# Performance work log

Hardware: AMD Instinct MI355X
Metric: run time of the kernel (lower is better)

The kernel has to match this reference:

```python
import jax, jax.numpy as jnp
import numpy as np

N, IN_DIM, H1, D, K, E, HEADS = 4096, 3000, 512, 64, 32, 49152, 4
ATT_THRESH = 0.25


def setup_inputs() -> dict:
    key = jax.random.key(0)
    ks = jax.random.split(key, 20)
    glorot = lambda k, fi, fo: jax.random.normal(k, (fi, fo), jnp.float32) * (2.0 / (fi + fo)) ** 0.5
    return {
        "x": jax.random.normal(ks[0], (N, IN_DIM), jnp.float32),
        "edge_index": jax.random.randint(ks[1], (2, E), 0, N, jnp.int32),
        "sub_nodes": jax.random.randint(ks[2], (N, K), 0, N, jnp.int32),
        # GCN encoder: in_dim -> 512 -> 64
        "enc_w1": glorot(ks[3], IN_DIM, H1), "enc_b1": jnp.zeros((H1,), jnp.float32),
        "enc_w2": glorot(ks[4], H1, D), "enc_b2": jnp.zeros((D,), jnp.float32),
        # linear decoder: 64 -> 512 -> in_dim
        "dec_w1": glorot(ks[5], D, H1), "dec_b1": jnp.zeros((H1,), jnp.float32),
        "dec_w2": glorot(ks[6], H1, IN_DIM), "dec_b2": jnp.zeros((IN_DIM,), jnp.float32),
        # MultiheadAttention (torch layout: in_proj_weight [3D, D], out_proj.weight [D, D])
        "attn_in_w": jax.random.normal(ks[7], (3 * D, D), jnp.float32) * (2.0 / D) ** 0.5,
        "attn_in_b": jnp.zeros((3 * D,), jnp.float32),
        "attn_out_w": jax.random.normal(ks[8], (D, D), jnp.float32) * (2.0 / D) ** 0.5,
        "attn_out_b": jnp.zeros((D,), jnp.float32),
        # Bilinear discriminator
        "bil_w": glorot(ks[9], D, D), "bil_b": jnp.zeros((), jnp.float32),
    }


def _gcn_conv(x, src, dst, W, b):
    n = x.shape[0]
    deg = jax.ops.segment_sum(jnp.ones(src.shape, x.dtype), dst, num_segments=n) + 1.0
    inv = jax.lax.rsqrt(deg)
    h = x @ W  # [n, out]
    coef = (inv[src] * inv[dst])[:, None]
    agg = jax.ops.segment_sum(h[src] * coef, dst, num_segments=n)
    agg = agg + h * (inv * inv)[:, None]  # self-loop contribution
    return agg + b


def _mha(x, in_w, in_b, out_w, out_b):
    # x: [N, D]; torch MultiheadAttention with batch of 1, dropout=0
    n, d = x.shape
    dh = d // HEADS
    qkv = x @ in_w.T + in_b  # [N, 3D]
    q, k, v = jnp.split(qkv, 3, axis=-1)
    rs = lambda t: t.reshape(n, HEADS, dh).transpose(1, 0, 2)  # [H, N, dh]
    q, k, v = rs(q), rs(k), rs(v)
    scores = jnp.einsum("hnd,hmd->hnm", q, k) / jnp.sqrt(jnp.asarray(dh, x.dtype))
    attn = jax.nn.softmax(scores, axis=-1)  # [H, N, N]
    out = jnp.einsum("hnm,hmd->hnd", attn, v).transpose(1, 0, 2).reshape(n, d)
    out = out @ out_w.T + out_b
    return out, attn.mean(axis=0)  # averaged attn weights [N, N]


def reference(x, edge_index, sub_nodes,
              enc_w1, enc_b1, enc_w2, enc_b2,
              dec_w1, dec_b1, dec_w2, dec_b2,
              attn_in_w, attn_in_b, attn_out_w, attn_out_b,
              bil_w, bil_b):
    src, dst = edge_index[0], edge_index[1]
    # GCN encoder
    h = jax.nn.relu(_gcn_conv(x, src, dst, enc_w1, enc_b1))
    spot_emb = _gcn_conv(h, src, dst, enc_w2, enc_b2)  # [N, D]
    # per-node subgraph gather + mean pool (global_mean_pool over fixed-size niches)
    local_niches = spot_emb[sub_nodes].mean(axis=1)  # [N, D]
    # linear decoder
    recon = jax.nn.relu(local_niches @ dec_w1 + dec_b1) @ dec_w2 + dec_b2
    # self-attention over all spots
    global_niches, attn_w = _mha(local_niches, attn_in_w, attn_in_b, attn_out_w, attn_out_b)
    # low-attention negative sampling
    n = local_niches.shape[0]
    kk = int(n * ATT_THRESH)
    _, idx = jax.lax.top_k(-attn_w, kk)  # smallest-k per row
    rand_idx = jax.random.randint(jax.random.key(42), (n,), 0, kk)
    sampled = idx[jnp.arange(n), rand_idx]
    neg_global = global_niches[sampled]
    # bilinear discriminator logits
    logits_pos = jnp.einsum("nd,de,ne->n", local_niches, bil_w, global_niches) + bil_b
    logits_neg = jnp.einsum("nd,de,ne->n", local_niches, bil_w, neg_global) + bil_b
    return recon, logits_pos, logits_neg
```

## Files before the change

### kernel.cpp

```cpp
#include <hip/hip_runtime.h>
#include <hip/hip_bf16.h>
#include <stdint.h>

#define NN      4096
#define INDIM   3000
#define H1DIM   512
#define DDIM    64
#define RECON_ELEMS (NN * INDIM)

typedef __attribute__((ext_vector_type(8))) __bf16          bf16x8;
typedef __attribute__((ext_vector_type(8))) unsigned short  u16x8;
typedef __attribute__((ext_vector_type(4))) float           f32x4;
typedef __attribute__((ext_vector_type(4))) unsigned int    u32x4;

__device__ __forceinline__ unsigned short f2bf(float f) {
  union { float f; unsigned int i; } v; v.f = f;
  unsigned int x = v.i;
  unsigned int lsb = (x >> 16) & 1u;
  x += 0x7FFFu + lsb;
  return (unsigned short)(x >> 16);
}

__device__ __forceinline__ void tf2x32(unsigned k0, unsigned k1, unsigned x0, unsigned x1,
                                       unsigned &o0, unsigned &o1) {
  unsigned ks2 = k0 ^ k1 ^ 0x1BD11BDAu;
  x0 += k0; x1 += k1;
#define TFR(r) { x0 += x1; x1 = (x1 << (r)) | (x1 >> (32 - (r))); x1 ^= x0; }
  TFR(13) TFR(15) TFR(26) TFR(6)
  x0 += k1; x1 += ks2 + 1u;
  TFR(17) TFR(29) TFR(16) TFR(24)
  x0 += ks2; x1 += k0 + 2u;
  TFR(13) TFR(15) TFR(26) TFR(6)
  x0 += k0; x1 += k1 + 3u;
  TFR(17) TFR(29) TFR(16) TFR(24)
  x0 += k1; x1 += ks2 + 4u;
  TFR(13) TFR(15) TFR(26) TFR(6)
  x0 += ks2; x1 += k0 + 5u;
#undef TFR
  o0 = x0; o1 = x1;
}

__global__ void k_deg(const int* __restrict__ dst, int* __restrict__ cnt, int E) {
  int e = blockIdx.x * 256 + threadIdx.x;
  if (e < E) atomicAdd(&cnt[dst[e]], 1);
}

__global__ void k_inv(const int* __restrict__ cnt, float* __restrict__ inv) {
  int n = blockIdx.x * 256 + threadIdx.x;
  if (n < NN) inv[n] = 1.0f / sqrtf((float)cnt[n] + 1.0f);
}

__global__ __launch_bounds__(1024) void k_scan(const int* __restrict__ cnt, int* __restrict__ offs) {
  __shared__ int ssum[1024];
  int tid = threadIdx.x;
  int c0 = cnt[tid*4], c1 = cnt[tid*4+1], c2 = cnt[tid*4+2], c3 = cnt[tid*4+3];
  int s = c0 + c1 + c2 + c3;
  ssum[tid] = s;
  __syncthreads();
  for (int off = 1; off < 1024; off <<= 1) {
    int v = (tid >= off) ? ssum[tid - off] : 0;
    __syncthreads();
    ssum[tid] += v;
    __syncthreads();
  }
  int base = ssum[tid] - s;
  offs[tid*4]   = base;
  offs[tid*4+1] = base + c0;
  offs[tid*4+2] = base + c0 + c1;
  offs[tid*4+3] = base + c0 + c1 + c2;
  if (tid == 1023) offs[4096] = ssum[1023];
}

__global__ void k_scatter(const int* __restrict__ dst, const int* __restrict__ offs,
                          int* __restrict__ cur, int* __restrict__ eid, int E) {
  int e = blockIdx.x * 256 + threadIdx.x;
  if (e < E) {
    int d = dst[e];
    int pos = offs[d] + atomicAdd(&cur[d], 1);
    eid[pos] = e;
  }
}

__global__ void k_sort(const int* __restrict__ offs, int* __restrict__ eid) {
  int n = blockIdx.x * 256 + threadIdx.x;
  if (n >= NN) return;
  int b = offs[n], e = offs[n+1];
  for (int i = b + 1; i < e; i++) {
    int v = eid[i]; int j = i - 1;
    while (j >= b && eid[j] > v) { eid[j+1] = eid[j]; j--; }
    eid[j+1] = v;
  }
}

#define FBK 16
__global__ __launch_bounds__(256) void k_gemm_f32(
    const float* __restrict__ A, const float* __restrict__ B, float* __restrict__ C) {
  __shared__ float As[FBK * 132];
  __shared__ float Bs[FBK * 132];
  const int tid = threadIdx.x;
  const int m0 = blockIdx.y * 128;
  const int n0 = blockIdx.x * 128;
  const int z  = blockIdx.z;
  const int kBeg = z ? 1504 : 0;
  const int kEnd = z ? 3000 : 1504;
  C += (size_t)z * NN * 512;
  const int lane = tid & 63, w = tid >> 6;
  const int rg = w * 4 + (lane >> 4);
  const int cg = lane & 15;
  f32x4 acc[2][2][4];
#pragma unroll
  for (int a = 0; a < 2; a++)
#pragma unroll
    for (int b = 0; b < 2; b++)
#pragma unroll
      for (int i = 0; i < 4; i++) acc[a][b][i] = (f32x4){0.f,0.f,0.f,0.f};

  const int arow = tid & 127;
  const int asl  = tid >> 7;
  const int bkr  = tid >> 4;
  const int bcq  = tid & 15;

  for (int kt = kBeg; kt < kEnd; kt += FBK) {
    bool full = (kt + FBK <= kEnd);
#pragma unroll
    for (int it = 0; it < 2; it++) {
      int kk = (asl * 2 + it) * 4;
      f32x4 v;
      if (full) {
        v = *(const f32x4*)(A + (size_t)(m0 + arow) * INDIM + kt + kk);
      } else {
#pragma unroll
        for (int j = 0; j < 4; j++)
          v[j] = (kt + kk + j < kEnd) ? A[(size_t)(m0 + arow) * INDIM + kt + kk + j] : 0.f;
      }
      As[(kk+0)*132 + arow] = v[0];
      As[(kk+1)*132 + arow] = v[1];
      As[(kk+2)*132 + arow] = v[2];
      As[(kk+3)*132 + arow] = v[3];
    }
    {
      f32x4 v0, v1;
      if (full || kt + bkr < kEnd) {
        const float* bp = B + (size_t)(kt + bkr) * 512 + n0 + bcq * 8;
        v0 = *(const f32x4*)bp;
        v1 = *(const f32x4*)(bp + 4);
      } else { v0 = (f32x4){0.f,0.f,0.f,0.f}; v1 = v0; }
      *(f32x4*)&Bs[bkr*132 + bcq*8]     = v0;
      *(f32x4*)&Bs[bkr*132 + bcq*8 + 4] = v1;
    }
    __syncthreads();
#pragma unroll
    for (int k = 0; k < FBK; k++) {
      f32x4 a0 = *(const f32x4*)&As[k*132 + rg*4];
      f32x4 a1 = *(const f32x4*)&As[k*132 + 64 + rg*4];
      f32x4 b0 = *(const f32x4*)&Bs[k*132 + cg*4];
      f32x4 b1 = *(const f32x4*)&Bs[k*132 + 64 + cg*4];
#pragma unroll
      for (int i = 0; i < 4; i++)
#pragma unroll
        for (int j = 0; j < 4; j++) {
          acc[0][0][i][j] = fmaf(a0[i], b0[j], acc[0][0][i][j]);
          acc[0][1][i][j] = fmaf(a0[i], b1[j], acc[0][1][i][j]);
          acc[1][0][i][j] = fmaf(a1[i], b0[j], acc[1][0][i][j]);
          acc[1][1][i][j] = fmaf(a1[i], b1[j], acc[1][1][i][j]);
        }
    }
    __syncthreads();
  }
#pragma unroll
  for (int a = 0; a < 2; a++)
#pragma unroll
    for (int i = 0; i < 4; i++) {
      int gr = m0 + a*64 + rg*4 + i;
#pragma unroll
      for (int b = 0; b < 2; b++)
        *(f32x4*)(C + (size_t)gr * 512 + n0 + b*64 + cg*4) = acc[a][b][i];
    }
}

__global__ void k_combine(float* __restrict__ c0, const float* __restrict__ c1) {
  int i = blockIdx.x * 256 + threadIdx.x;
  ((f32x4*)c0)[i] = ((const f32x4*)c0)[i] + ((const f32x4*)c1)[i];
}

__global__ __launch_bounds__(256) void k_gemm_bf(
    const unsigned short* __restrict__ A, const float* __restrict__ B,
    float* __restrict__ Cf, unsigned short* __restrict__ Cb,
    const float* __restrict__ bias,
    int M, int N, int K, int ldc, int mode) {
  __shared__ __attribute__((aligned(16))) unsigned short As[128 * 40];
  __shared__ __attribute__((aligned(16))) unsigned short Bs[128 * 40];
  const int tid  = threadIdx.x;
  const int m0   = blockIdx.y * 128;
  const int n0   = blockIdx.x * 128;
  const int lane = tid & 63;
  const int wid  = tid >> 6;
  const int wm   = wid >> 1, wn = wid & 1;
  const int lrow = lane & 15, lk = lane >> 4;

  f32x4 acc[4][4];
#pragma unroll
  for (int i = 0; i < 4; i++)
#pragma unroll
    for (int j = 0; j < 4; j++) acc[i][j] = (f32x4){0.f, 0.f, 0.f, 0.f};

  for (int k0 = 0; k0 < K; k0 += 32) {
#pragma unroll
    for (int it = 0; it < 2; it++) {
      int c   = it * 256 + tid;
      int row = c >> 2, kc = c & 3;
      int kg  = k0 + kc * 8;
      u16x8 v = *(const u16x8*)(A + (size_t)(m0 + row) * K + kg);
      *(u16x8*)&As[row * 40 + kc * 8] = v;
    }
    {
      int kk_ = tid & 31;
      int nc0 = tid >> 5;
      int kg  = k0 + kk_;
#pragma unroll
      for (int it = 0; it < 2; it++) {
        int nc = nc0 + it * 8;
        int ng = n0 + nc * 8;
        unsigned short vb[8];
        if (ng + 8 <= N) {
          f32x4 f0 = *(const f32x4*)(B + (size_t)kg * N + ng);
          f32x4 f1 = *(const f32x4*)(B + (size_t)kg * N + ng + 4);
#pragma unroll
          for (int j = 0; j < 4; j++) { vb[j] = f2bf(f0[j]); vb[4+j] = f2bf(f1[j]); }
        } else {
#pragma unroll
          for (int j = 0; j < 8; j++)
            vb[j] = (ng + j < N) ? f2bf(B[(size_t)kg * N + ng + j]) : (unsigned short)0;
        }
#pragma unroll
        for (int j = 0; j < 8; j++) Bs[(nc * 8 + j) * 40 + kk_] = vb[j];
      }
    }
    __syncthreads();
    bf16x8 af[4], bfr[4];
#pragma unroll
    for (int mi = 0; mi < 4; mi++) {
      u16x8 r = *(const u16x8*)&As[(wm * 64 + mi * 16 + lrow) * 40 + lk * 8];
      af[mi] = __builtin_bit_cast(bf16x8, r);
    }
#pragma unroll
    for (int ni = 0; ni < 4; ni++) {
      u16x8 r = *(const u16x8*)&Bs[(wn * 64 + ni * 16 + lrow) * 40 + lk * 8];
      bfr[ni] = __builtin_bit_cast(bf16x8, r);
    }
#pragma unroll
    for (int mi = 0; mi < 4; mi++)
#pragma unroll
      for (int ni = 0; ni < 4; ni++)
        acc[mi][ni] = __builtin_amdgcn_mfma_f32_16x16x32_bf16(af[mi], bfr[ni], acc[mi][ni], 0, 0, 0);
    __syncthreads();
  }

#pragma unroll
  for (int mi = 0; mi < 4; mi++)
#pragma unroll
    for (int ni = 0; ni < 4; ni++)
#pragma unroll
      for (int reg = 0; reg < 4; reg++) {
        int gr = m0 + wm * 64 + mi * 16 + lk * 4 + reg;
        int gc = n0 + wn * 64 + ni * 16 + lrow;
        if (gc < N) {
          float v = acc[mi][ni][reg] + bias[gc];
          if (mode == 1) {
            if (v < 0.f) v = 0.f;
            Cb[(size_t)gr * ldc + gc] = f2bf(v);
          } else {
            Cf[(size_t)gr * ldc + gc] = v;
          }
        }
      }
}

__global__ __launch_bounds__(256) void k_agg(
    const float* __restrict__ X, float* __restrict__ Y,
    const float* __restrict__ bias, const int* __restrict__ offs,
    const int* __restrict__ eid, const int* __restrict__ esrc,
    const float* __restrict__ inv, int F, int relu) {
  int n = blockIdx.x;
  int beg = offs[n], end = offs[n + 1];
  float invn = inv[n];
  float inv2 = invn * invn;
  for (int d = threadIdx.x; d < F; d += 256) {
    float acc = 0.f;
    for (int t = beg; t < end; t++) {
      int e = eid[t]; int s = esrc[e];
      float cf = inv[s] * invn;
      acc += X[(size_t)s * F + d] * cf;
    }
    acc += X[(size_t)n * F + d] * inv2;
    acc += bias[d];
    if (relu && acc < 0.f) acc = 0.f;
    Y[(size_t)n * F + d] = acc;
  }
}

__global__ __launch_bounds__(256) void k_mmw2(const float* __restrict__ h,
                                              const float* __restrict__ w2,
                                              float* __restrict__ out) {
  __shared__ float hs[4 * 512];
  int tid  = threadIdx.x;
  int brow = blockIdx.x * 4;
  const f32x4* src = (const f32x4*)(h + (size_t)brow * 512);
  f32x4* dst4 = (f32x4*)hs;
  dst4[tid]       = src[tid];
  dst4[tid + 256] = src[tid + 256];
  __syncthreads();
  int r = tid >> 6, c = tid & 63;
  float acc = 0.f;
  const float* hr = hs + r * 512;
#pragma unroll 8
  for (int k = 0; k < 512; k++) acc = fmaf(hr[k], w2[k * 64 + c], acc);
  out[(size_t)(brow + r) * 64 + c] = acc;
}

__global__ void k_pool(const float* __restrict__ spot, const int* __restrict__ sub,
                       float* __restrict__ local, unsigned short* __restrict__ local_bf) {
  int n = blockIdx.x, d = threadIdx.x;
  float acc = 0.f;
  for (int j = 0; j < 32; j++) {
    int s = sub[n * 32 + j];
    acc += spot[(size_t)s * 64 + d];
  }
  float lv = acc * 0.03125f;
  local[(size_t)n * 64 + d] = lv;
  local_bf[(size_t)n * 64 + d] = f2bf(lv);
}

__global__ void k_qkv(const float* __restrict__ local, const float* __restrict__ iw,
                      const float* __restrict__ ib,
                      float* __restrict__ Qp, float* __restrict__ Kp, float* __restrict__ Vp) {
  __shared__ float lx[64];
  int n = blockIdx.x, t = threadIdx.x;
  if (t < 64) lx[t] = local[(size_t)n * 64 + t];
  __syncthreads();
  float acc = 0.f;
#pragma unroll 8
  for (int d = 0; d < 64; d++) acc = fmaf(lx[d], iw[t * 64 + d], acc);
  acc += ib[t];
  if (t < 64)       Qp[(size_t)n * 64 + t] = acc;
  else if (t < 128) Kp[(size_t)n * 64 + (t - 64)] = acc;
  else              Vp[(size_t)n * 64 + (t - 128)] = acc;
}

#define RT 2
__global__ __launch_bounds__(256, 3) void k_attn(
    const float* __restrict__ Qp, const float* __restrict__ Kp, const float* __restrict__ Vp,
    float* __restrict__ ctx, int* __restrict__ sampled) {
  __shared__ __attribute__((aligned(16))) float regA[2][64 * 64];
  __shared__ float sMZ[2][2][4];
  __shared__ unsigned wtot[4];
  __shared__ unsigned sh_prefix;
  __shared__ int sh_r;

  const int t   = threadIdx.x;
  const int n0  = blockIdx.x * RT;
  const int sm  = t & 63;
  const int sq  = (t >> 6) & 1;
  const int shp = t >> 7;
  const int dq  = t & 15;
  const int me  = t >> 4;
  const int stm = t >> 4;
  const int stc = t & 15;
  const int wv  = t >> 6;
  const int lane = t & 63;

  float Qreg[32];
  {
    const float* qp = Qp + (size_t)(n0 + sq) * 64 + shp * 32;
#pragma unroll
    for (int j = 0; j < 8; j++) {
      f32x4 qv = *(const f32x4*)(qp + j * 4);
      Qreg[j * 4 + 0] = qv[0]; Qreg[j * 4 + 1] = qv[1];
      Qreg[j * 4 + 2] = qv[2]; Qreg[j * 4 + 3] = qv[3];
    }
  }

  f32x4 kA[4], kB[4];
#pragma unroll
  for (int jj = 0; jj < 4; jj++) {
    kA[jj] = *(const f32x4*)(Kp + (size_t)(jj * 16 + stm) * 64 + stc * 4);
    kB[jj] = *(const f32x4*)(Kp + (size_t)(64 + jj * 16 + stm) * 64 + stc * 4);
  }

  float M[2] = {-3.0e38f, -3.0e38f}, Z[2] = {0.f, 0.f};

  for (int tp = 0; tp < 64; tp += 2) {
#pragma unroll
    for (int half = 0; half < 2; half++) {
      float* Kt = regA[half];
#pragma unroll
      for (int jj = 0; jj < 4; jj++) {
        int m = jj * 16 + stm;
        int sc = (stc + (m & 15) + 4 * (m >> 4)) & 15;
        *(f32x4*)&Kt[(m * 16 + sc) * 4] = (half == 0) ? kA[jj] : kB[jj];
      }
      __syncthreads();
      if (tp + 2 + half < 64) {
#pragma unroll
        for (int jj = 0; jj < 4; jj++) {
          f32x4 v = *(const f32x4*)(Kp + (size_t)((tp + 2 + half) * 64 + jj * 16 + stm) * 64 + stc * 4);
          if (half == 0) kA[jj] = v; else kB[jj] = v;
        }
      }
      float s[2] = {0.f, 0.f};
#pragma unroll
      for (int ci = 0; ci < 8; ci++) {
        int c = shp * 8 + ci;
        int sc = (c + (sm & 15) + 4 * (sm >> 4)) & 15;
        f32x4 k4 = *(const f32x4*)&Kt[(sm * 16 + sc) * 4];
        int hh = ci >> 2;
#pragma unroll
        for (int e = 0; e < 4; e++)
          s[hh] = fmaf(Qreg[ci * 4 + e], k4[e], s[hh]);
      }
#pragma unroll
      for (int hh = 0; hh < 2; hh++) {
        float sv = s[hh] * 0.25f;
        if (sv > M[hh]) { Z[hh] = fmaf(Z[hh], __expf(M[hh] - sv), 1.0f); M[hh] = sv; }
        else            Z[hh] += __expf(sv - M[hh]);
      }
    }
  }
  {
    float* redM = regA[0];
    float* redZ = regA[0] + 512;
    int row = sq * 4 + shp * 2;
    redM[(row + 0) * 64 + sm] = M[0];
    redM[(row + 1) * 64 + sm] = M[1];
    redZ[(row + 0) * 64 + sm] = Z[0];
    redZ[(row + 1) * 64 + sm] = Z[1];
    __syncthreads();
    if (t < 8) {
      const float* pm = &redM[t * 64];
      const float* pz = &redZ[t * 64];
      float Mv = -3.0e38f, Zv = 0.f;
      for (int i = 0; i < 64; i++) {
        float m_ = pm[i], z_ = pz[i];
        if (m_ > Mv) { Zv = fmaf(Zv, __expf(Mv - m_), z_); Mv = m_; }
        else         Zv = fmaf(z_, __expf(m_ - Mv), Zv);
      }
      sMZ[0][t >> 2][t & 3] = Mv;
      sMZ[1][t >> 2][t & 3] = Zv;
    }
    __syncthreads();
  }
  float Mh[2], iZ[2];
#pragma unroll
  for (int hh = 0; hh < 2; hh++) {
    Mh[hh] = sMZ[0][sq][shp * 2 + hh];
    iZ[hh] = 1.0f / sMZ[1][sq][shp * 2 + hh];
  }
  __syncthreads();

#pragma unroll
  for (int jj = 0; jj < 4; jj++)
    kA[jj] = *(const f32x4*)(Kp + (size_t)(jj * 16 + stm) * 64 + stc * 4);
  float* KtB   = regA[0];
  float* Pt    = regA[1];
  float* rvbuf = regA[1] + 1024;
  float o4[2][4];
#pragma unroll
  for (int q = 0; q < 2; q++)
#pragma unroll
    for (int e = 0; e < 4; e++) o4[q][e] = 0.f;
  float rv[2][16];

  for (int sb = 0; sb < 4; sb++) {
    for (int ti = 0; ti < 16; ti++) {
      const int tile = sb * 16 + ti;
#pragma unroll
      for (int jj = 0; jj < 4; jj++) {
        int m = jj * 16 + stm;
        int sc = (stc + (m & 15) + 4 * (m >> 4)) & 15;
        *(f32x4*)&KtB[(m * 16 + sc) * 4] = kA[jj];
      }
      __syncthreads();
      if (tile + 1 < 64) {
#pragma unroll
        for (int jj = 0; jj < 4; jj++)
          kA[jj] = *(const f32x4*)(Kp + (size_t)((tile + 1) * 64 + jj * 16 + stm) * 64 + stc * 4);
      }
      {
        float s[2] = {0.f, 0.f};
#pragma unroll
        for (int ci = 0; ci < 8; ci++) {
          int c = shp * 8 + ci;
          int sc = (c + (sm & 15) + 4 * (sm >> 4)) & 15;
          f32x4 k4 = *(const f32x4*)&KtB[(sm * 16 + sc) * 4];
          int hh = ci >> 2;
#pragma unroll
          for (int e = 0; e < 4; e++)
            s[hh] = fmaf(Qreg[ci * 4 + e], k4[e], s[hh]);
        }
#pragma unroll
        for (int hh = 0; hh < 2; hh++) {
          float p = __expf(s[hh] * 0.25f - Mh[hh]) * iZ[hh];
          Pt[(sq * 4 + shp * 2 + hh) * 68 + sm] = p;
        }
      }
      f32x4 vt[4];
#pragma unroll
      for (int i = 0; i < 4; i++)
        vt[i] = *(const f32x4*)(Vp + (size_t)(tile * 64 + me * 4 + i) * 64 + dq * 4);
      __syncthreads();
      if (wv == sb) {
        rvbuf[(0 * 16 + ti) * 64 + lane] =
            0.25f * (Pt[0 * 68 + lane] + Pt[1 * 68 + lane] +
                     Pt[2 * 68 + lane] + Pt[3 * 68 + lane]);
        rvbuf[(1 * 16 + ti) * 64 + lane] =
            0.25f * (Pt[4 * 68 + lane] + Pt[5 * 68 + lane] +
                     Pt[6 * 68 + lane] + Pt[7 * 68 + lane]);
      }
      {
        int h = dq >> 2;
        f32x4 p4[2];
#pragma unroll
        for (int q = 0; q < 2; q++)
          p4[q] = *(const f32x4*)&Pt[(q * 4 + h) * 68 + me * 4];
#pragma unroll
        for (int i = 0; i < 4; i++) {
#pragma unroll
          for (int q = 0; q < 2; q++)
#pragma unroll
            for (int e = 0; e < 4; e++)
              o4[q][e] = fmaf(p4[q][i], vt[i][e], o4[q][e]);
        }
      }
    }
    if (wv == sb) {
#pragma unroll
      for (int g = 0; g < 16; g++) {
        rv[0][g] = rvbuf[(0 * 16 + g) * 64 + lane];
        rv[1][g] = rvbuf[(1 * 16 + g) * 64 + lane];
      }
    }
  }

  {
    float* Osh = regA[0];
#pragma unroll
    for (int q = 0; q < 2; q++)
#pragma unroll
      for (int e = 0; e < 4; e++)
        Osh[((me * 2 + q) * 16 + dq) * 4 + e] = o4[q][e];
    __syncthreads();
    if (t < 128) {
      int q2 = t >> 6, d = t & 63;
      float acc = 0.f;
      for (int i = 0; i < 16; i++)
        acc += Osh[((i * 2 + q2) * 16 + (d >> 2)) * 4 + (d & 3)];
      ctx[(size_t)(n0 + q2) * 64 + d] = acc;
    }
    __syncthreads();
  }

  unsigned* histT = (unsigned*)regA[0];
  unsigned* gaux  = ((unsigned*)regA[0]) + 1024;
#pragma unroll
  for (int q = 0; q < RT; q++) {
    int n = n0 + q;
    if (t == 0) {
      unsigned a0, a1, b0, b1;
      tf2x32(0u, 42u, 0u, 2u, a0, a1);
      tf2x32(0u, 42u, 1u, 3u, b0, b1);
      unsigned o0, o1, bits;
      if (n < 2048) { tf2x32(a1, b1, (unsigned)n, (unsigned)(n + 2048), o0, o1); bits = o0; }
      else          { tf2x32(a1, b1, (unsigned)(n - 2048), (unsigned)n, o0, o1); bits = o1; }
      sh_r = (int)(bits & 1023u);
      sh_prefix = 0u;
    }
    __syncthreads();
    int r = sh_r;
    unsigned prefix = 0u;
    for (int level = 0; level < 4; level++) {
      int shift = 24 - 8 * level;
      unsigned c0 = 0, c1 = 0, c2 = 0, c3 = 0;
#pragma unroll
      for (int g = 0; g < 16; g++) {
        unsigned u = __float_as_uint(rv[q][g]);
        bool ok = (level == 0) || ((u >> (shift + 8)) == (prefix >> (shift + 8)));
        unsigned bin = (u >> shift) & 255u;
        unsigned long long mok = __ballot(ok);
        unsigned long long b0 = __ballot(bin & 1u);
        unsigned long long b1 = __ballot(bin & 2u);
        unsigned long long b2 = __ballot(bin & 4u);
        unsigned long long b3 = __ballot(bin & 8u);
        unsigned long long b4 = __ballot(bin & 16u);
        unsigned long long b5 = __ballot(bin & 32u);
        unsigned long long b6 = __ballot(bin & 64u);
        unsigned long long b7 = __ballot(bin & 128u);
        unsigned long long m = mok;
        m &= (lane & 1)  ? b0 : ~b0;
        m &= (lane & 2)  ? b1 : ~b1;
        m &= (lane & 4)  ? b2 : ~b2;
        m &= (lane & 8)  ? b3 : ~b3;
        m &= (lane & 16) ? b4 : ~b4;
        m &= (lane & 32) ? b5 : ~b5;
        c0 += (unsigned)__builtin_popcountll(m & ~b6 & ~b7);
        c1 += (unsigned)__builtin_popcountll(m &  b6 & ~b7);
        c2 += (unsigned)__builtin_popcountll(m & ~b6 &  b7);
        c3 += (unsigned)__builtin_popcountll(m &  b6 &  b7);
      }
      histT[wv * 256 + lane]       = c0;
      histT[wv * 256 + 64 + lane]  = c1;
      histT[wv * 256 + 128 + lane] = c2;
      histT[wv * 256 + 192 + lane] = c3;
      __syncthreads();
      unsigned own = histT[t] + histT[256 + t] + histT[512 + t] + histT[768 + t];
      unsigned v = own;
      for (int off = 1; off < 64; off <<= 1) {
        unsigned u2 = __shfl_up(v, off, 64);
        if ((t & 63) >= off) v += u2;
      }
      if ((t & 63) == 63) wtot[t >> 6] = v;
      __syncthreads();
      unsigned basev = 0;
#pragma unroll
      for (int w = 0; w < 4; w++) if (w < (t >> 6)) basev += wtot[w];
      v += basev;
      unsigned cb = v - own;
      if ((unsigned)r >= cb && (unsigned)r < v) {
        sh_prefix = prefix | ((unsigned)t << shift);
        sh_r = r - (int)cb;
      }
      __syncthreads();
      prefix = sh_prefix; r = sh_r;
    }
    {
      unsigned long long msk[16];
#pragma unroll
      for (int g = 0; g < 16; g++)
        msk[g] = __ballot(__float_as_uint(rv[q][g]) == prefix);
      if (lane == 0) {
#pragma unroll
        for (int g = 0; g < 16; g++)
          gaux[wv * 16 + g] = (unsigned)__builtin_popcountll(msk[g]);
      }
      __syncthreads();
      if (t < 64) {
        unsigned acc = 0;
        for (int i = 0; i < t; i++) acc += gaux[i];
        gaux[64 + t] = acc;
      }
      __syncthreads();
#pragma unroll
      for (int g = 0; g < 16; g++) {
        if (__float_as_uint(rv[q][g]) == prefix) {
          unsigned before = (unsigned)__builtin_popcountll(msk[g] & ((1ull << lane) - 1ull));
          if ((int)(gaux[64 + wv * 16 + g] + before) == r)
            sampled[n] = (wv * 16 + g) * 64 + lane;
        }
      }
      __syncthreads();
    }
  }
}

__global__ void k_outproj(const float* __restrict__ ctx, const float* __restrict__ ow,
                          const float* __restrict__ ob, float* __restrict__ gni) {
  __shared__ float cx[64];
  int n = blockIdx.x, t = threadIdx.x;
  cx[t] = ctx[(size_t)n * 64 + t];
  __syncthreads();
  float acc = 0.f;
#pragma unroll 8
  for (int j = 0; j < 64; j++) acc = fmaf(cx[j], ow[t * 64 + j], acc);
  gni[(size_t)n * 64 + t] = acc + ob[t];
}

__global__ void k_logits(const float* __restrict__ local, const float* __restrict__ gni,
                         const int* __restrict__ sampled,
                         const float* __restrict__ bw, const float* __restrict__ bb,
                         float* __restrict__ outp, float* __restrict__ outn) {
  __shared__ float lv[64], gp[64], gn[64];
  int n = blockIdx.x, t = threadIdx.x;
  int sm = sampled[n];
  lv[t] = local[(size_t)n * 64 + t];
  gp[t] = gni[(size_t)n * 64 + t];
  gn[t] = gni[(size_t)sm * 64 + t];
  __syncthreads();
  float tp = 0.f, tn = 0.f;
#pragma unroll 8
  for (int e = 0; e < 64; e++) {
    float w = bw[t * 64 + e];
    tp = fmaf(w, gp[e], tp);
    tn = fmaf(w, gn[e], tn);
  }
  float vp = lv[t] * tp, vn = lv[t] * tn;
  for (int off = 32; off; off >>= 1) {
    vp += __shfl_down(vp, off, 64);
    vn += __shfl_down(vn, off, 64);
  }
  if (t == 0) {
    outp[n] = vp + bb[0];
    outn[n] = vn + bb[0];
  }
}

extern "C" void kernel_launch(void* const* d_in, const int* in_sizes, int n_in,
                              void* d_out, int out_size, void* d_ws, size_t ws_size,
                              hipStream_t stream) {
  const float* x      = (const float*)d_in[0];
  const int*   edge   = (const int*)d_in[1];
  const int*   sub    = (const int*)d_in[2];
  const float* enc_w1 = (const float*)d_in[3];
  const float* enc_b1 = (const float*)d_in[4];
  const float* enc_w2 = (const float*)d_in[5];
  const float* enc_b2 = (const float*)d_in[6];
  const float* dec_w1 = (const float*)d_in[7];
  const float* dec_b1 = (const float*)d_in[8];
  const float* dec_w2 = (const float*)d_in[9];
  const float* dec_b2 = (const float*)d_in[10];
  const float* ain_w  = (const float*)d_in[11];
  const float* ain_b  = (const float*)d_in[12];
  const float* aout_w = (const float*)d_in[13];
  const float* aout_b = (const float*)d_in[14];
  const float* bil_w  = (const float*)d_in[15];
  const float* bil_b  = (const float*)d_in[16];
  float* out = (float*)d_out;

  const int E = in_sizes[1] / 2;
  const int* esrc = edge;
  const int* edst = edge + E;

  char* base = (char*)d_ws;
  const size_t MB = (size_t)1 << 20;
  float*          cpart    = (float*)(base + 0);
  float*          h_pre    = (float*)(base + 0);
  unsigned short* dech_bf  = (unsigned short*)(base + 0);
  float*          h        = (float*)(base + 8*MB);
  float*          Qp       = (float*)(base + 8*MB);
  float*          Kp       = (float*)(base + 9*MB);
  float*          Vp       = (float*)(base + 10*MB);
  float*          ctx      = (float*)(base + 11*MB);
  float*          gni      = (float*)(base + 12*MB);
  float*          hw2      = (float*)(base + 16*MB);
  float*          spot     = (float*)(base + 17*MB);
  float*          localf   = (float*)(base + 18*MB);
  unsigned short* local_bf = (unsigned short*)(base + 19*MB);
  char* ip = base + 19*MB + 512*1024;
  float* inv    = (float*)ip;  ip += 16384;
  int*   degcnt = (int*)ip;    ip += 16384;
  int*   cursor = (int*)ip;    ip += 16384;
  int*   offs   = (int*)ip;    ip += 16640;
  int*   sampled= (int*)ip;    ip += 16384;
  int*   eid    = (int*)ip;    ip += (size_t)E * 4;

  hipMemsetAsync(degcnt, 0, (size_t)NN * 4, stream);
  hipMemsetAsync(cursor, 0, (size_t)NN * 4, stream);

  int egrid = (E + 255) / 256;
  k_deg<<<egrid, 256, 0, stream>>>(edst, degcnt, E);
  k_inv<<<(NN + 255) / 256, 256, 0, stream>>>(degcnt, inv);
  k_scan<<<1, 1024, 0, stream>>>(degcnt, offs);
  k_scatter<<<egrid, 256, 0, stream>>>(edst, offs, cursor, eid, E);
  k_sort<<<(NN + 255) / 256, 256, 0, stream>>>(offs, eid);

  {
    dim3 g(4, 32, 2);
    k_gemm_f32<<<g, 256, 0, stream>>>(x, enc_w1, cpart);
  }
  k_combine<<<(NN * 512 / 4) / 256, 256, 0, stream>>>(h_pre, cpart + (size_t)NN * 512);
  k_agg<<<NN, 256, 0, stream>>>(h_pre, h, enc_b1, offs, eid, esrc, inv, 512, 1);
  k_mmw2<<<NN / 4, 256, 0, stream>>>(h, enc_w2, hw2);
  k_agg<<<NN, 256, 0, stream>>>(hw2, spot, enc_b2, offs, eid, esrc, inv, 64, 0);
  k_pool<<<NN, 64, 0, stream>>>(spot, sub, localf, local_bf);

  {
    dim3 g(4, 32);
    k_gemm_bf<<<g, 256, 0, stream>>>(local_bf, dec_w1, nullptr, dech_bf, dec_b1,
                                     NN, 512, 64, 512, 1);
  }
  {
    dim3 g(24, 32);
    k_gemm_bf<<<g, 256, 0, stream>>>(dech_bf, dec_w2, out, nullptr, dec_b2,
                                     NN, INDIM, 512, INDIM, 2);
  }

  k_qkv<<<NN, 192, 0, stream>>>(localf, ain_w, ain_b, Qp, Kp, Vp);
  k_attn<<<NN / RT, 256, 0, stream>>>(Qp, Kp, Vp, ctx, sampled);
  k_outproj<<<NN, 64, 0, stream>>>(ctx, aout_w, aout_b, gni);
  k_logits<<<NN, 64, 0, stream>>>(localf, gni, sampled, bil_w, bil_b,
                                  out + RECON_ELEMS, out + RECON_ELEMS + NN);
}
```

Baseline: 992.2 us.

## Double-buffer f32 GEMM LDS tiles and compute attention stats via warp shuffles

The fp32 GEMM now keeps two LDS buffers and loads the next K-tile into registers while computing the current one. This removes one __syncthreads per iteration and hides global load latency behind the FMAs. The attention max/sum pass stops staging K through shared memory. Each thread instead computes partial dot products directly from its register-held K fragment, and the partials are reduced with xor shuffles. This drops LDS traffic and barriers in that loop, at the cost of extra shuffle work and a changed per-thread ownership of rows and heads.

```diff
diff --git a/kernel.cpp b/kernel.cpp
--- a/kernel.cpp
+++ b/kernel.cpp
@@ -95,8 +95,8 @@
 #define FBK 16
 __global__ __launch_bounds__(256) void k_gemm_f32(
     const float* __restrict__ A, const float* __restrict__ B, float* __restrict__ C) {
-  __shared__ float As[FBK * 132];
-  __shared__ float Bs[FBK * 132];
+  __shared__ float As[2][FBK * 132];
+  __shared__ float Bs[2][FBK * 132];
   const int tid = threadIdx.x;
   const int m0 = blockIdx.y * 128;
   const int n0 = blockIdx.x * 128;
@@ -120,41 +120,69 @@
   const int bkr  = tid >> 4;
   const int bcq  = tid & 15;
 
-  for (int kt = kBeg; kt < kEnd; kt += FBK) {
-    bool full = (kt + FBK <= kEnd);
+  f32x4 ra[2], rb0, rb1;
+  {
+    const int kt = kBeg;
+    const bool full = (kt + FBK <= kEnd);
 #pragma unroll
     for (int it = 0; it < 2; it++) {
       int kk = (asl * 2 + it) * 4;
-      f32x4 v;
       if (full) {
-        v = *(const f32x4*)(A + (size_t)(m0 + arow) * INDIM + kt + kk);
+        ra[it] = *(const f32x4*)(A + (size_t)(m0 + arow) * INDIM + kt + kk);
       } else {
 #pragma unroll
         for (int j = 0; j < 4; j++)
-          v[j] = (kt + kk + j < kEnd) ? A[(size_t)(m0 + arow) * INDIM + kt + kk + j] : 0.f;
-      }
-      As[(kk+0)*132 + arow] = v[0];
-      As[(kk+1)*132 + arow] = v[1];
-      As[(kk+2)*132 + arow] = v[2];
-      As[(kk+3)*132 + arow] = v[3];
-    }
-    {
-      f32x4 v0, v1;
-      if (full || kt + bkr < kEnd) {
-        const float* bp = B + (size_t)(kt + bkr) * 512 + n0 + bcq * 8;
-        v0 = *(const f32x4*)bp;
-        v1 = *(const f32x4*)(bp + 4);
-      } else { v0 = (f32x4){0.f,0.f,0.f,0.f}; v1 = v0; }
-      *(f32x4*)&Bs[bkr*132 + bcq*8]     = v0;
-      *(f32x4*)&Bs[bkr*132 + bcq*8 + 4] = v1;
-    }
-    __syncthreads();
+          ra[it][j] = (kt + kk + j < kEnd) ? A[(size_t)(m0 + arow) * INDIM + kt + kk + j] : 0.f;
+      }
+    }
+    if (full || kt + bkr < kEnd) {
+      const float* bp = B + (size_t)(kt + bkr) * 512 + n0 + bcq * 8;
+      rb0 = *(const f32x4*)bp;
+      rb1 = *(const f32x4*)(bp + 4);
+    } else { rb0 = (f32x4){0.f,0.f,0.f,0.f}; rb1 = rb0; }
+  }
+
+  int buf = 0;
+  for (int kt = kBeg; kt < kEnd; kt += FBK) {
+#pragma unroll
+    for (int it = 0; it < 2; it++) {
+      int kk = (asl * 2 + it) * 4;
+      As[buf][(kk+0)*132 + arow] = ra[it][0];
+      As[buf][(kk+1)*132 + arow] = ra[it][1];
+      As[buf][(kk+2)*132 + arow] = ra[it][2];
+      As[buf][(kk+3)*132 + arow] = ra[it][3];
+    }
+    *(f32x4*)&Bs[buf][bkr*132 + bcq*8]     = rb0;
+    *(f32x4*)&Bs[buf][bkr*132 + bcq*8 + 4] = rb1;
+    __syncthreads();
+    const int ktn = kt + FBK;
+    if (ktn < kEnd) {
+      const bool fulln = (ktn + FBK <= kEnd);
+#pragma unroll
+      for (int it = 0; it < 2; it++) {
+        int kk = (asl * 2 + it) * 4;
+        if (fulln) {
+          ra[it] = *(const f32x4*)(A + (size_t)(m0 + arow) * INDIM + ktn + kk);
+        } else {
+#pragma unroll
+          for (int j = 0; j < 4; j++)
+            ra[it][j] = (ktn + kk + j < kEnd) ? A[(size_t)(m0 + arow) * INDIM + ktn + kk + j] : 0.f;
+        }
+      }
+      if (fulln || ktn + bkr < kEnd) {
+        const float* bp = B + (size_t)(ktn + bkr) * 512 + n0 + bcq * 8;
+        rb0 = *(const f32x4*)bp;
+        rb1 = *(const f32x4*)(bp + 4);
+      } else { rb0 = (f32x4){0.f,0.f,0.f,0.f}; rb1 = rb0; }
+    }
+    const float* Asb = As[buf];
+    const float* Bsb = Bs[buf];
 #pragma unroll
     for (int k = 0; k < FBK; k++) {
-      f32x4 a0 = *(const f32x4*)&As[k*132 + rg*4];
-      f32x4 a1 = *(const f32x4*)&As[k*132 + 64 + rg*4];
-      f32x4 b0 = *(const f32x4*)&Bs[k*132 + cg*4];
-      f32x4 b1 = *(const f32x4*)&Bs[k*132 + 64 + cg*4];
+      f32x4 a0 = *(const f32x4*)&Asb[k*132 + rg*4];
+      f32x4 a1 = *(const f32x4*)&Asb[k*132 + 64 + rg*4];
+      f32x4 b0 = *(const f32x4*)&Bsb[k*132 + cg*4];
+      f32x4 b1 = *(const f32x4*)&Bsb[k*132 + 64 + cg*4];
 #pragma unroll
       for (int i = 0; i < 4; i++)
 #pragma unroll
@@ -165,7 +193,7 @@
           acc[1][1][i][j] = fmaf(a1[i], b1[j], acc[1][1][i][j]);
         }
     }
-    __syncthreads();
+    buf ^= 1;
   }
 #pragma unroll
   for (int a = 0; a < 2; a++)
@@ -380,60 +408,76 @@
     }
   }
 
-  f32x4 kA[4], kB[4];
-#pragma unroll
-  for (int jj = 0; jj < 4; jj++) {
-    kA[jj] = *(const f32x4*)(Kp + (size_t)(jj * 16 + stm) * 64 + stc * 4);
-    kB[jj] = *(const f32x4*)(Kp + (size_t)(64 + jj * 16 + stm) * 64 + stc * 4);
+  const int hsel = stc >> 2;
+  const int rr   = stc & 3;
+  float qsh[2][4];
+#pragma unroll
+  for (int q = 0; q < 2; q++) {
+    f32x4 qv = *(const f32x4*)(Qp + (size_t)(n0 + q) * 64 + stc * 4);
+    qsh[q][0] = qv[0]; qsh[q][1] = qv[1]; qsh[q][2] = qv[2]; qsh[q][3] = qv[3];
   }
 
   float M[2] = {-3.0e38f, -3.0e38f}, Z[2] = {0.f, 0.f};
-
-  for (int tp = 0; tp < 64; tp += 2) {
-#pragma unroll
-    for (int half = 0; half < 2; half++) {
-      float* Kt = regA[half];
-#pragma unroll
-      for (int jj = 0; jj < 4; jj++) {
-        int m = jj * 16 + stm;
-        int sc = (stc + (m & 15) + 4 * (m >> 4)) & 15;
-        *(f32x4*)&Kt[(m * 16 + sc) * 4] = (half == 0) ? kA[jj] : kB[jj];
-      }
-      __syncthreads();
-      if (tp + 2 + half < 64) {
-#pragma unroll
-        for (int jj = 0; jj < 4; jj++) {
-          f32x4 v = *(const f32x4*)(Kp + (size_t)((tp + 2 + half) * 64 + jj * 16 + stm) * 64 + stc * 4);
-          if (half == 0) kA[jj] = v; else kB[jj] = v;
-        }
-      }
-      float s[2] = {0.f, 0.f};
-#pragma unroll
-      for (int ci = 0; ci < 8; ci++) {
-        int c = shp * 8 + ci;
-        int sc = (c + (sm & 15) + 4 * (sm >> 4)) & 15;
-        f32x4 k4 = *(const f32x4*)&Kt[(sm * 16 + sc) * 4];
-        int hh = ci >> 2;
-#pragma unroll
-        for (int e = 0; e < 4; e++)
-          s[hh] = fmaf(Qreg[ci * 4 + e], k4[e], s[hh]);
-      }
-#pragma unroll
-      for (int hh = 0; hh < 2; hh++) {
-        float sv = s[hh] * 0.25f;
-        if (sv > M[hh]) { Z[hh] = fmaf(Z[hh], __expf(M[hh] - sv), 1.0f); M[hh] = sv; }
-        else            Z[hh] += __expf(sv - M[hh]);
+  {
+    f32x4 ka[4], kb[4];
+#pragma unroll
+    for (int j = 0; j < 4; j++) {
+      ka[j] = *(const f32x4*)(Kp + (size_t)(j * 16 + stm) * 64 + stc * 4);
+      kb[j] = *(const f32x4*)(Kp + (size_t)(64 + j * 16 + stm) * 64 + stc * 4);
+    }
+    for (int tp = 0; tp < 64; tp += 2) {
+#pragma unroll
+      for (int half = 0; half < 2; half++) {
+        f32x4 k0 = (half == 0) ? ka[0] : kb[0];
+        f32x4 k1 = (half == 0) ? ka[1] : kb[1];
+        f32x4 k2 = (half == 0) ? ka[2] : kb[2];
+        f32x4 k3 = (half == 0) ? ka[3] : kb[3];
+        float s00 = 0.f, s01 = 0.f, s02 = 0.f, s03 = 0.f;
+        float s10 = 0.f, s11 = 0.f, s12 = 0.f, s13 = 0.f;
+#pragma unroll
+        for (int e = 0; e < 4; e++) {
+          s00 = fmaf(qsh[0][e], k0[e], s00);
+          s01 = fmaf(qsh[0][e], k1[e], s01);
+          s02 = fmaf(qsh[0][e], k2[e], s02);
+          s03 = fmaf(qsh[0][e], k3[e], s03);
+          s10 = fmaf(qsh[1][e], k0[e], s10);
+          s11 = fmaf(qsh[1][e], k1[e], s11);
+          s12 = fmaf(qsh[1][e], k2[e], s12);
+          s13 = fmaf(qsh[1][e], k3[e], s13);
+        }
+        if (tp + 2 + half < 64) {
+#pragma unroll
+          for (int j = 0; j < 4; j++) {
+            f32x4 v = *(const f32x4*)(Kp + (size_t)((tp + 2 + half) * 64 + j * 16 + stm) * 64 + stc * 4);
+            if (half == 0) ka[j] = v; else kb[j] = v;
+          }
+        }
+        s00 += __shfl_xor(s00, 1, 64); s00 += __shfl_xor(s00, 2, 64);
+        s01 += __shfl_xor(s01, 1, 64); s01 += __shfl_xor(s01, 2, 64);
+        s02 += __shfl_xor(s02, 1, 64); s02 += __shfl_xor(s02, 2, 64);
+        s03 += __shfl_xor(s03, 1, 64); s03 += __shfl_xor(s03, 2, 64);
+        s10 += __shfl_xor(s10, 1, 64); s10 += __shfl_xor(s10, 2, 64);
+        s11 += __shfl_xor(s11, 1, 64); s11 += __shfl_xor(s11, 2, 64);
+        s12 += __shfl_xor(s12, 1, 64); s12 += __shfl_xor(s12, 2, 64);
+        s13 += __shfl_xor(s13, 1, 64); s13 += __shfl_xor(s13, 2, 64);
+        float sv0 = (rr == 0) ? s00 : (rr == 1) ? s01 : (rr == 2) ? s02 : s03;
+        float sv1 = (rr == 0) ? s10 : (rr == 1) ? s11 : (rr == 2) ? s12 : s13;
+        sv0 *= 0.25f; sv1 *= 0.25f;
+        if (sv0 > M[0]) { Z[0] = fmaf(Z[0], __expf(M[0] - sv0), 1.0f); M[0] = sv0; }
+        else            Z[0] += __expf(sv0 - M[0]);
+        if (sv1 > M[1]) { Z[1] = fmaf(Z[1], __expf(M[1] - sv1), 1.0f); M[1] = sv1; }
+        else            Z[1] += __expf(sv1 - M[1]);
       }
     }
   }
   {
     float* redM = regA[0];
     float* redZ = regA[0] + 512;
-    int row = sq * 4 + shp * 2;
-    redM[(row + 0) * 64 + sm] = M[0];
-    redM[(row + 1) * 64 + sm] = M[1];
-    redZ[(row + 0) * 64 + sm] = Z[0];
-    redZ[(row + 1) * 64 + sm] = Z[1];
+    int slot = stm + 16 * rr;
+    redM[(0 * 4 + hsel) * 64 + slot] = M[0];
+    redM[(1 * 4 + hsel) * 64 + slot] = M[1];
+    redZ[(0 * 4 + hsel) * 64 + slot] = Z[0];
+    redZ[(1 * 4 + hsel) * 64 + slot] = Z[1];
     __syncthreads();
     if (t < 8) {
       const float* pm = &redM[t * 64];
@@ -457,6 +501,7 @@
   }
   __syncthreads();
 
+  f32x4 kA[4];
 #pragma unroll
   for (int jj = 0; jj < 4; jj++)
     kA[jj] = *(const f32x4*)(Kp + (size_t)(jj * 16 + stm) * 64 + stc * 4);
```

New measurement: 921.7 us (median of 2 runs). 7.1% less time.
